# Optimization experiments

Hardware: AMD Instinct MI355X
Metric: run time of the kernel (lower is better)

Reference implementation:

```python
import jax, jax.numpy as jnp
import numpy as np
import math

N, E, C, NB, NEL, NG = 8192, 131072, 64, 8, 4, 16
R_MAX, AVG_NEI, P_CUT, NL, SH = 5.0, 16.0, 6, 2, 16


def _sph(u):
    # real spherical harmonics l=0..3, component normalization (sum_m Y_lm^2 = 2l+1 on unit sphere)
    x, y, z = u[:, 0], u[:, 1], u[:, 2]
    s3, s15, s5 = math.sqrt(3.0), math.sqrt(15.0), math.sqrt(5.0)
    s105, s7 = math.sqrt(105.0), math.sqrt(7.0)
    c35, c21 = math.sqrt(35.0 / 8.0), math.sqrt(21.0 / 8.0)
    Y = [jnp.ones_like(x),
         s3 * x, s3 * y, s3 * z,
         s15 * x * y, s15 * y * z, 0.5 * s5 * (3 * z * z - 1), s15 * x * z, 0.5 * s15 * (x * x - y * y),
         c35 * y * (3 * x * x - y * y), s105 * x * y * z, c21 * y * (5 * z * z - 1),
         0.5 * s7 * (5 * z ** 3 - 3 * z), c21 * x * (5 * z * z - 1),
         0.5 * s105 * z * (x * x - y * y), c35 * x * (x * x - 3 * y * y)]
    return jnp.stack(Y, axis=-1)  # [E,16]


def _bessel(r):
    k = jnp.arange(1, NB + 1, dtype=r.dtype)
    return math.sqrt(2.0 / R_MAX) * jnp.sin(k * jnp.pi * r[:, None] / R_MAX) / r[:, None]


def _poly_cutoff(r):
    p = float(P_CUT)
    x = r / R_MAX
    f = (1.0 - 0.5 * (p + 1) * (p + 2) * x ** p + p * (p + 2) * x ** (p + 1)
         - 0.5 * p * (p + 1) * x ** (p + 2))
    return f * (x < 1.0)


def setup_inputs() -> dict:
    key = jax.random.key(0)
    ks = jax.random.split(key, 16)
    sc = lambda fan: 1.0 / math.sqrt(fan)
    return {
        "pos": 2.0 * jax.random.normal(ks[0], (N, 3), jnp.float32),
        "atom_types": jax.random.randint(ks[1], (N,), 0, NEL),
        "edge_index": jax.random.randint(ks[2], (2, E), 0, N),
        "batch": jnp.sort(jax.random.randint(ks[3], (N,), 0, NG)),
        "W_embed": jax.random.normal(ks[4], (NEL, C), jnp.float32),
        "W_r1": sc(NB) * jax.random.normal(ks[5], (NL, NB, 64), jnp.float32),
        "W_r2": sc(64) * jax.random.normal(ks[6], (NL, 64, 64), jnp.float32),
        "W_r3": sc(64) * jax.random.normal(ks[7], (NL, 64, C), jnp.float32),
        "W_sc": sc(C) * jax.random.normal(ks[8], (NL, NEL, C, C), jnp.float32),
        "w_prod": 0.5 * jax.random.normal(ks[9], (NL, NEL, 4), jnp.float32),
        "w_ro0": sc(C) * jax.random.normal(ks[10], (C,), jnp.float32),
        "W_ro1a": sc(C) * jax.random.normal(ks[11], (C, 16), jnp.float32),
        "w_ro1b": sc(16) * jax.random.normal(ks[12], (16,), jnp.float32),
    }


def reference(pos, atom_types, edge_index, batch, W_embed, W_r1, W_r2, W_r3,
              W_sc, w_prod, w_ro0, W_ro1a, w_ro1b):
    src, dst = edge_index[0], edge_index[1]
    vec = pos[dst] - pos[src]                      # [E,3]
    r = jnp.sqrt(jnp.sum(vec * vec, -1) + 1e-12)   # [E]
    Y = _sph(vec / r[:, None])                     # [E,SH]
    edge_feats = _bessel(r) * _poly_cutoff(r)[:, None]  # [E,NB]
    h = W_embed[atom_types]                        # one-hot @ W == lookup, [N,C]
    energies = [jnp.zeros((NG,), pos.dtype)]       # pair_repulsion disabled
    for i in range(NL):
        Rw = jax.nn.silu(edge_feats @ W_r1[i])
        Rw = jax.nn.silu(Rw @ W_r2[i])
        Rw = Rw @ W_r3[i]                          # radial MLP weights [E,C]
        # gather-TP-scatter: message [E,C,SH] -> node A [N,C,SH]
        m = (Rw * h[src])[:, :, None] * Y[:, None, :]
        A = jax.ops.segment_sum(m.reshape(E, C * SH), dst,
                                num_segments=N).reshape(N, C, SH) / AVG_NEI
        sc_feat = jnp.einsum('nc,ncd->nd', h, W_sc[i][atom_types])  # element-dep skip
        inv = jnp.stack([A[:, :, 0],
                         jnp.sum(A[:, :, 1:4] ** 2, -1),
                         jnp.sum(A[:, :, 4:9] ** 2, -1),
                         jnp.sum(A[:, :, 9:16] ** 2, -1)], axis=-1)  # [N,C,4]
        h = jnp.einsum('ncj,nj->nc', inv, w_prod[i][atom_types]) + sc_feat
        if i < NL - 1:
            e_node = h @ w_ro0                     # linear readout
        else:
            e_node = jax.nn.silu(h @ W_ro1a) @ w_ro1b  # gated MLP readout
        energies.append(jax.ops.segment_sum(e_node, batch, num_segments=NG))
    contributions = jnp.stack(energies, -1)        # [NG, NL+1]
    return jnp.sum(contributions, -1)              # total energy per graph
```

## Files before the change

kernel.cpp:

```cpp
#include <hip/hip_runtime.h>
#include <hip/hip_bf16.h>
#include <math.h>

#define N_NODES 8192
#define N_EDGES 131072
#define NGRP 16
#define NLAY 2
#define NELM 4
constexpr float INV_AVG = 1.0f / 16.0f;
constexpr float PI_F = 3.14159265358979323846f;

#define CV_POS   0
#define CV_EMB   24576
#define CV_SC    42240
#define CV_PROD  75008
#define CV_RO0   75040
#define CV_RO1A  75104
#define CV_RO1B  76128
#define CVT_N    76144

#define SWZ_PER_L 10240
#define SWZ_N     20480

#define B_CVT  230
#define B_SWZ  80
#define B_HIST 512
#define CVT_WORK 58736

#define GU_GRID 4096

typedef __hip_bfloat16 bf16;
typedef __attribute__((ext_vector_type(8))) short bf16x8;
typedef __attribute__((ext_vector_type(4))) float f32x4;

__device__ __forceinline__ float silu_f(float x){ return x / (1.0f + __expf(-x)); }
__device__ __forceinline__ float bfbits2f(unsigned short u){
  return __uint_as_float(((unsigned)u) << 16);
}
__device__ __forceinline__ void unpack2(unsigned u, float& lo, float& hi){
  lo = __uint_as_float(u << 16);
  hi = __uint_as_float(u & 0xffff0000u);
}
__device__ __forceinline__ short f2bs(float v){
  union { bf16 b; short s; } u; u.b = __float2bfloat16(v); return u.s;
}
__device__ __forceinline__ float ldf(const void* p, int i, int flag){
  if (flag) return bfbits2f(((const unsigned short*)p)[i]);
  return ((const float*)p)[i];
}
__device__ __forceinline__ int detect_fl(const void* pos){
  int lane = threadIdx.x & 63;
  const unsigned short* u = (const unsigned short*)pos;
  float va = bfbits2f(u[2*lane]), vb = bfbits2f(u[2*lane+1]);
  bool bad = !(fabsf(va) <= 1000.0f) || !(fabsf(vb) <= 1000.0f);
  return (__ballot(bad) == 0ull) ? 1 : 0;
}
__device__ __forceinline__ void WSYNC(){ __builtin_amdgcn_wave_barrier(); }

__device__ __forceinline__ void gl_lds4(const void* g, void* l){
  __builtin_amdgcn_global_load_lds(
      (const __attribute__((address_space(1))) unsigned*)g,
      (__attribute__((address_space(3))) unsigned*)l, 4, 0, 0);
}

__global__ void k_setup1(const void* __restrict__ pos, const void* __restrict__ Wemb,
                         const void* __restrict__ Wsc, const void* __restrict__ wprod,
                         const void* __restrict__ wro0, const void* __restrict__ Wro1a,
                         const void* __restrict__ wro1b, const void* __restrict__ Wr1,
                         const void* __restrict__ Wr2, const void* __restrict__ Wr3,
                         const int* __restrict__ dstp, float* __restrict__ cv,
                         short* __restrict__ swz, int* __restrict__ deg){
  int b = blockIdx.x, tix = threadIdx.x;
  if (b >= B_CVT + B_SWZ){
    int e = (b - B_CVT - B_SWZ)*256 + tix;
    atomicAdd(&deg[dstp[e]], 1);
    return;
  }
  int fl = detect_fl(pos);
  if (b < B_CVT){
    int i = b*256 + tix;
    if (i < 24576){ cv[CV_POS + i] = ldf(pos, i, fl); return; }
    if (i < 24832){ int j=i-24576; cv[CV_EMB + j] = ldf(Wemb, j, fl); return; }
    if (i < 57600){ int j=i-24832; cv[CV_SC  + j] = ldf(Wsc,  j, fl); return; }
    if (i < 57632){ int j=i-57600; cv[CV_PROD+ j] = ldf(wprod,j, fl); return; }
    if (i < 57696){ int j=i-57632; cv[CV_RO0 + j] = ldf(wro0, j, fl); return; }
    if (i < 58720){ int j=i-57696; cv[CV_RO1A+ j] = ldf(Wro1a,j, fl); return; }
    if (i < CVT_WORK){ int j=i-58720; cv[CV_RO1B+ j] = ldf(wro1b,j, fl); return; }
    return;
  }
  int i = (b - B_CVT)*256 + tix;
  int l = i / SWZ_PER_L, w = i % SWZ_PER_L;
  float v;
  if (w < 2048){
    int t = w >> 9, q = (w >> 7) & 3, n = (w >> 3) & 15, j = w & 7;
    int k = q*8 + j;
    v = (k < 8) ? ldf(Wr1, l*512 + k*64 + t*16 + n, fl) : 0.0f;
  } else if (w < 6144){
    int w2 = w - 2048;
    int nt = w2 >> 10, kt = (w2 >> 9) & 1, q = (w2 >> 7) & 3, n = (w2 >> 3) & 15, j = w2 & 7;
    int k = kt*32 + q*8 + j;
    v = ldf(Wr2, l*4096 + k*64 + nt*16 + n, fl);
  } else {
    int w3 = w - 6144;
    int nt = w3 >> 10, kt = (w3 >> 9) & 1, q = (w3 >> 7) & 3, n = (w3 >> 3) & 15, j = w3 & 7;
    int k = kt*32 + q*8 + j;
    v = ldf(Wr3, l*4096 + k*64 + nt*16 + n, fl);
  }
  swz[i] = f2bs(v);
}

__global__ void k_scan(const int* __restrict__ deg, int* __restrict__ row_start,
                       int* __restrict__ cursor, float* __restrict__ ene2){
  __shared__ int lds[1024];
  int t = threadIdx.x;
  if (t < 8*NGRP) ene2[t] = 0.0f;
  int v[8]; int tot = 0;
#pragma unroll
  for (int k = 0; k < 8; k++){ v[k] = deg[t*8+k]; tot += v[k]; }
  lds[t] = tot; __syncthreads();
  for (int off = 1; off < 1024; off <<= 1){
    int x = (t >= off) ? lds[t-off] : 0;
    __syncthreads();
    lds[t] += x;
    __syncthreads();
  }
  int base = lds[t] - tot;
#pragma unroll
  for (int k = 0; k < 8; k++){ row_start[t*8+k] = base; cursor[t*8+k] = base; base += v[k]; }
  if (t == 1023) row_start[N_NODES] = base;
}

__global__ void k_fillgeom(const int* __restrict__ ei, int* __restrict__ cursor,
                           const float* __restrict__ posf, const int* __restrict__ types,
                           int* __restrict__ sslot, unsigned char* __restrict__ tsl,
                           unsigned short* __restrict__ Yb, float* __restrict__ rbuf){
  int e = blockIdx.x*256 + threadIdx.x;
  int s = ei[e], d = ei[N_EDGES + e];
  int slot = atomicAdd(&cursor[d], 1);
  sslot[slot] = s;
  tsl[slot] = (unsigned char)types[s];
  float vx = posf[d*3+0] - posf[s*3+0];
  float vy = posf[d*3+1] - posf[s*3+1];
  float vz = posf[d*3+2] - posf[s*3+2];
  float r = sqrtf(vx*vx + vy*vy + vz*vz + 1e-12f);
  float ir = 1.0f / r;
  float x = vx*ir, y = vy*ir, z = vz*ir;
  const float s3 = 1.7320508075688772f, s15 = 3.872983346207417f, s5 = 2.23606797749979f;
  const float s105 = 10.246950765959598f, s7 = 2.6457513110645907f;
  const float c35 = 2.091650066335189f, c21 = 1.6201851746019651f;
  float x2 = x*x, y2 = y*y, z2 = z*z;
  float ys[16] = {
    1.0f, s3*x, s3*y, s3*z,
    s15*x*y, s15*y*z, 0.5f*s5*(3.0f*z2-1.0f), s15*x*z,
    0.5f*s15*(x2-y2), c35*y*(3.0f*x2-y2), s105*x*y*z, c21*y*(5.0f*z2-1.0f),
    0.5f*s7*(5.0f*z2*z-3.0f*z), c21*x*(5.0f*z2-1.0f), 0.5f*s105*z*(x2-y2),
    c35*x*(x2-3.0f*y2) };
  union { bf16 b[16]; uint4 u[2]; } pk;
#pragma unroll
  for (int k = 0; k < 16; k++) pk.b[k] = __float2bfloat16(ys[k]);
  uint4* yp = (uint4*)(Yb + (size_t)slot*16);
  yp[0] = pk.u[0];
  yp[1] = pk.u[1];
  rbuf[slot] = r;
}

#define ROWS 72
template<int LAYER_KIND>
__global__ void __launch_bounds__(64) k_gu(const short* __restrict__ sw,
        const float* __restrict__ rbuf, const unsigned char* __restrict__ tsl,
        const int* __restrict__ sslot, const float* __restrict__ h_old,
        float* __restrict__ h_new, const unsigned short* __restrict__ Yb,
        const int* __restrict__ row_start, const int* __restrict__ types,
        const float* __restrict__ Wsc, const float* __restrict__ wprod,
        const float* __restrict__ wemb, const float* __restrict__ wro0,
        const float* __restrict__ Wro1a, const float* __restrict__ wro1b,
        const int* __restrict__ batch, float* __restrict__ ene2){
  __shared__ __align__(16) short A_[16*ROWS];
  __shared__ __align__(16) float hS[LAYER_KIND ? 16 : 1][64];
  __shared__ __align__(16) unsigned short yS[16][16];
  __shared__ float hn_l[64];
  int lane = threadIdx.x;
  int q = lane >> 4, nn = lane & 15;
  short* A = A_;

  const bf16x8* S1 = (const bf16x8*)(sw);
  const bf16x8* S2 = (const bf16x8*)(sw + 2048);
  const bf16x8* S3 = (const bf16x8*)(sw + 6144);

  float e0=0.f, e1=0.f, e2=0.f, e3=0.f;
  if (LAYER_KIND == 0){
    e0 = wemb[lane]; e1 = wemb[64+lane]; e2 = wemb[128+lane]; e3 = wemb[192+lane];
  }

  for (int n = blockIdx.x; n < N_NODES; n += GU_GRID){
    int beg = row_start[n], end = row_start[n + 1];

    float acc[16];
#pragma unroll
    for (int s = 0; s < 16; s++) acc[s] = 0.0f;

    for (int cb = beg; cb < end; cb += 16){
      int cnt = min(16, end - cb);
      WSYNC();
      const char* ysrc = (const char*)Yb + (size_t)cb*32 + lane*4;
      gl_lds4(ysrc,       &yS[0][0]);
      gl_lds4(ysrc + 256, &yS[8][0]);
      int tv = 0;
      if (LAYER_KIND == 0){
        tv = (int)tsl[min(cb + nn, N_EDGES - 1)];
      } else {
        int sv = sslot[min(cb + nn, N_EDGES - 1)];
        for (int i = 0; i < cnt; i++){
          int src = __builtin_amdgcn_readlane(sv, i);
          gl_lds4(h_old + (size_t)src*64 + lane, &hS[i][0]);
        }
      }
      {
        float r = rbuf[min(cb + nn, N_EDGES - 1)];
        float xc = r * 0.2f;
        float f = 0.0f;
        if (xc < 1.0f){
          float x3 = xc*xc*xc, x6 = x3*x3, x7 = x6*xc, x8 = x7*xc;
          f = 1.0f - 28.0f*x6 + 48.0f*x7 - 21.0f*x8;
        }
        float bs = 0.6324555320336759f * f / r;
        float t0 = PI_F * r * 0.2f;
        bf16x8 af1 = {0,0,0,0,0,0,0,0};
        if (q == 0){
#pragma unroll
          for (int j = 0; j < 8; j++) af1[j] = f2bs(bs * __sinf((float)(j+1) * t0));
        }
        f32x4 macc[4];
#pragma unroll
        for (int t = 0; t < 4; t++){
          bf16x8 b = S1[t*64 + q*16 + nn];
          f32x4 z = {0.f,0.f,0.f,0.f};
          macc[t] = __builtin_amdgcn_mfma_f32_16x16x32_bf16(af1, b, z, 0, 0, 0);
        }
#pragma unroll
        for (int t = 0; t < 4; t++)
#pragma unroll
          for (int rg = 0; rg < 4; rg++)
            A[(q*4+rg)*ROWS + t*16 + nn] = f2bs(silu_f(macc[t][rg]));
        WSYNC();
        bf16x8 a0 = *(const bf16x8*)&A[nn*ROWS + 0*32 + q*8];
        bf16x8 a1 = *(const bf16x8*)&A[nn*ROWS + 1*32 + q*8];
        WSYNC();
#pragma unroll
        for (int t = 0; t < 4; t++){
          f32x4 z = {0.f,0.f,0.f,0.f};
          bf16x8 b0 = S2[t*128 + 0*64 + q*16 + nn];
          bf16x8 b1 = S2[t*128 + 1*64 + q*16 + nn];
          z = __builtin_amdgcn_mfma_f32_16x16x32_bf16(a0, b0, z, 0, 0, 0);
          z = __builtin_amdgcn_mfma_f32_16x16x32_bf16(a1, b1, z, 0, 0, 0);
          macc[t] = z;
        }
#pragma unroll
        for (int t = 0; t < 4; t++)
#pragma unroll
          for (int rg = 0; rg < 4; rg++)
            A[(q*4+rg)*ROWS + t*16 + nn] = f2bs(silu_f(macc[t][rg]));
        WSYNC();
        a0 = *(const bf16x8*)&A[nn*ROWS + 0*32 + q*8];
        a1 = *(const bf16x8*)&A[nn*ROWS + 1*32 + q*8];
        WSYNC();
#pragma unroll
        for (int t = 0; t < 4; t++){
          f32x4 z = {0.f,0.f,0.f,0.f};
          bf16x8 b0 = S3[t*128 + 0*64 + q*16 + nn];
          bf16x8 b1 = S3[t*128 + 1*64 + q*16 + nn];
          z = __builtin_amdgcn_mfma_f32_16x16x32_bf16(a0, b0, z, 0, 0, 0);
          z = __builtin_amdgcn_mfma_f32_16x16x32_bf16(a1, b1, z, 0, 0, 0);
          macc[t] = z;
        }
#pragma unroll
        for (int t = 0; t < 4; t++)
#pragma unroll
          for (int rg = 0; rg < 4; rg++)
            A[(q*4+rg)*ROWS + t*16 + nn] = f2bs(macc[t][rg]);
        WSYNC();
      }
      asm volatile("s_waitcnt vmcnt(0)" ::: "memory");
      __builtin_amdgcn_sched_barrier(0);
      for (int i = 0; i < cnt; i++){
        float rw = bfbits2f((unsigned short)A[i*ROWS + lane]);
        float hv;
        if (LAYER_KIND == 0){
          int ty = __builtin_amdgcn_readlane(tv, i);
          hv = (ty & 2) ? ((ty & 1) ? e3 : e2) : ((ty & 1) ? e1 : e0);
        } else {
          hv = hS[i][lane];
        }
        float g = rw * hv;
        const uint4* yq = (const uint4*)&yS[i][0];
        uint4 ya = yq[0], yb = yq[1];
        float lo, hi;
        unpack2(ya.x, lo, hi); acc[0]  += g*lo; acc[1]  += g*hi;
        unpack2(ya.y, lo, hi); acc[2]  += g*lo; acc[3]  += g*hi;
        unpack2(ya.z, lo, hi); acc[4]  += g*lo; acc[5]  += g*hi;
        unpack2(ya.w, lo, hi); acc[6]  += g*lo; acc[7]  += g*hi;
        unpack2(yb.x, lo, hi); acc[8]  += g*lo; acc[9]  += g*hi;
        unpack2(yb.y, lo, hi); acc[10] += g*lo; acc[11] += g*hi;
        unpack2(yb.z, lo, hi); acc[12] += g*lo; acc[13] += g*hi;
        unpack2(yb.w, lo, hi); acc[14] += g*lo; acc[15] += g*hi;
      }
    }
#pragma unroll
    for (int s = 0; s < 16; s++) acc[s] *= INV_AVG;

    int ty = __builtin_amdgcn_readfirstlane(types[n]);
    const float* Ws = Wsc + (size_t)ty*4096;
    const float* hrow = (LAYER_KIND == 0) ? (wemb + ty*64) : (h_old + (size_t)n*64);
    float sc0 = 0.f, sc1 = 0.f, sc2 = 0.f, sc3 = 0.f;
#pragma unroll
    for (int c = 0; c < 64; c += 4){
      sc0 += hrow[c+0] * Ws[(c+0)*64 + lane];
      sc1 += hrow[c+1] * Ws[(c+1)*64 + lane];
      sc2 += hrow[c+2] * Ws[(c+2)*64 + lane];
      sc3 += hrow[c+3] * Ws[(c+3)*64 + lane];
    }
    float sc = (sc0 + sc1) + (sc2 + sc3);

    float inv0 = acc[0];
    float inv1 = acc[1]*acc[1] + acc[2]*acc[2] + acc[3]*acc[3];
    float inv2 = acc[4]*acc[4] + acc[5]*acc[5] + acc[6]*acc[6] + acc[7]*acc[7]
               + acc[8]*acc[8];
    float inv3 = acc[9]*acc[9] + acc[10]*acc[10] + acc[11]*acc[11] + acc[12]*acc[12]
               + acc[13]*acc[13] + acc[14]*acc[14] + acc[15]*acc[15];
    const float* wp = wprod + ty*4;
    float hn = inv0*wp[0] + inv1*wp[1] + inv2*wp[2] + inv3*wp[3] + sc;
    if (LAYER_KIND == 0)
      h_new[(size_t)n*64 + lane] = hn;

    float ev;
    if (LAYER_KIND == 0){
      float p = hn * wro0[lane];
#pragma unroll
      for (int off = 32; off >= 1; off >>= 1) p += __shfl_xor(p, off, 64);
      ev = p;
    } else {
      WSYNC();
      hn_l[lane] = hn;
      WSYNC();
      int j = lane & 15;
      float pj = 0.0f;
#pragma unroll
      for (int c = 0; c < 64; c++)
        pj += hn_l[c] * Wro1a[c*16 + j];
      float evj = silu_f(pj) * wro1b[j];
      evj += __shfl_xor(evj, 8, 64);
      evj += __shfl_xor(evj, 4, 64);
      evj += __shfl_xor(evj, 2, 64);
      evj += __shfl_xor(evj, 1, 64);
      ev = evj;
    }
    if (lane == 0) atomicAdd(&ene2[(n & 7)*NGRP + batch[n]], ev);
  }
}

__global__ void k_out(const float* __restrict__ ene2, const void* __restrict__ pos,
                      void* __restrict__ out){
  int fl = detect_fl(pos);
  int t = threadIdx.x;
  if (t < NGRP){
    float v = 0.0f;
#pragma unroll
    for (int k = 0; k < 8; k++) v += ene2[k*NGRP + t];
    if (fl) ((bf16*)out)[t] = __float2bfloat16(v);
    else    ((float*)out)[t] = v;
  }
}

static inline size_t rup(size_t x){ return (x + 255) & ~(size_t)255; }

extern "C" void kernel_launch(void* const* d_in, const int* in_sizes, int n_in,
                              void* d_out, int out_size, void* d_ws, size_t ws_size,
                              hipStream_t stream) {
  const void* pos   = d_in[0];
  const int*  types = (const int*)d_in[1];
  const int*  ei    = (const int*)d_in[2];
  const int*  batch = (const int*)d_in[3];
  const void* Wemb  = d_in[4];
  const void* Wr1   = d_in[5];
  const void* Wr2   = d_in[6];
  const void* Wr3   = d_in[7];
  const void* Wsc   = d_in[8];
  const void* wprod = d_in[9];
  const void* wro0  = d_in[10];
  const void* Wro1a = d_in[11];
  const void* wro1b = d_in[12];

  char* w = (char*)d_ws;
  float* cv       = (float*)w; w += rup((size_t)CVT_N*4);
  short* swz      = (short*)w; w += rup((size_t)SWZ_N*2);
  float* ene2     = (float*)w; w += 512;
  int*   deg      = (int*)  w; w += rup((size_t)N_NODES*4);
  int*   row_start= (int*)  w; w += rup((size_t)(N_NODES+1)*4);
  int*   cursor   = (int*)  w; w += rup((size_t)N_NODES*4);
  int*   sslot    = (int*)  w; w += rup((size_t)N_EDGES*4);
  unsigned char* tsl = (unsigned char*)w; w += rup((size_t)N_EDGES);
  float* hbuf     = (float*)w; w += rup((size_t)N_NODES*64*4);
  float* rbuf     = (float*)w; w += rup((size_t)N_EDGES*4);
  unsigned short* Yb = (unsigned short*)w; w += rup((size_t)N_EDGES*16*2);
  w += 4096;

  hipMemsetAsync(deg, 0, N_NODES*4, stream);

  const int* dstp = ei + N_EDGES;
  k_setup1<<<B_CVT + B_SWZ + B_HIST, 256, 0, stream>>>(
      pos, Wemb, Wsc, wprod, wro0, Wro1a, wro1b, Wr1, Wr2, Wr3, dstp, cv, swz, deg);
  k_scan<<<1, 1024, 0, stream>>>(deg, row_start, cursor, ene2);
  k_fillgeom<<<N_EDGES/256, 256, 0, stream>>>(ei, cursor, cv + CV_POS, types,
      sslot, tsl, Yb, rbuf);

  k_gu<0><<<GU_GRID, 64, 0, stream>>>(swz, rbuf, tsl, sslot,
      hbuf , hbuf , Yb, row_start, types,
      cv + CV_SC, cv + CV_PROD, cv + CV_EMB,
      cv + CV_RO0, cv + CV_RO1A, cv + CV_RO1B, batch, ene2);
  k_gu<1><<<GU_GRID, 64, 0, stream>>>(swz + SWZ_PER_L, rbuf, tsl, sslot,
      hbuf , hbuf , Yb, row_start, types,
      cv + CV_SC + (size_t)NELM*4096, cv + CV_PROD + NELM*4, cv + CV_EMB,
      cv + CV_RO0, cv + CV_RO1A, cv + CV_RO1B, batch, ene2);

  k_out<<<1, 64, 0, stream>>>(ene2, pos, d_out);
}
```

Baseline: 201.4 us.

## Interleave two nodes per block to overlap gathers and MFMA chains

Each block now handles two nodes, n and n+GU_GRID, in lockstep. It double-buffers the LDS tiles (A, hS, yS) so one node's gathers and radial-MLP MFMAs are issued alongside the other's, which gives the scheduler independent work to hide memory and MFMA latency. The change assumes the grid covers exactly half of the nodes, because the grid-stride loop is gone. It also doubles LDS and accumulator register use, and a node with more edges leaves the other slot idle while it finishes.

```diff
diff --git a/kernel.cpp b/kernel.cpp
--- a/kernel.cpp
+++ b/kernel.cpp
@@ -165,6 +165,165 @@
 }
 
 #define ROWS 72
+
+template<int LK>
+__device__ __forceinline__ int issueA(const unsigned short* Yb,
+    const unsigned char* tsl, const int* sslot, const float* h_old,
+    int cb, int cnt, int lane, int nn,
+    unsigned short (*yS)[16], float (*hS)[64]){
+  const char* ysrc = (const char*)Yb + (size_t)cb*32 + lane*4;
+  gl_lds4(ysrc,       &yS[0][0]);
+  gl_lds4(ysrc + 256, &yS[8][0]);
+  int tv = 0;
+  if (LK == 0){
+    tv = (int)tsl[min(cb + nn, N_EDGES - 1)];
+  } else {
+    int sv = sslot[min(cb + nn, N_EDGES - 1)];
+    for (int i = 0; i < cnt; i++){
+      int src = __builtin_amdgcn_readlane(sv, i);
+      gl_lds4(h_old + (size_t)src*64 + lane, &hS[i][0]);
+    }
+  }
+  return tv;
+}
+
+__device__ __forceinline__ void mlp_s1(const bf16x8* S1, short* A,
+    const float* rbuf, int cb, int q, int nn){
+  float r = rbuf[min(cb + nn, N_EDGES - 1)];
+  float xc = r * 0.2f;
+  float f = 0.0f;
+  if (xc < 1.0f){
+    float x3 = xc*xc*xc, x6 = x3*x3, x7 = x6*xc, x8 = x7*xc;
+    f = 1.0f - 28.0f*x6 + 48.0f*x7 - 21.0f*x8;
+  }
+  float bs = 0.6324555320336759f * f / r;
+  float t0 = PI_F * r * 0.2f;
+  bf16x8 af1 = {0,0,0,0,0,0,0,0};
+  if (q == 0){
+#pragma unroll
+    for (int j = 0; j < 8; j++) af1[j] = f2bs(bs * __sinf((float)(j+1) * t0));
+  }
+  f32x4 macc[4];
+#pragma unroll
+  for (int t = 0; t < 4; t++){
+    bf16x8 b = S1[t*64 + q*16 + nn];
+    f32x4 z = {0.f,0.f,0.f,0.f};
+    macc[t] = __builtin_amdgcn_mfma_f32_16x16x32_bf16(af1, b, z, 0, 0, 0);
+  }
+#pragma unroll
+  for (int t = 0; t < 4; t++)
+#pragma unroll
+    for (int rg = 0; rg < 4; rg++)
+      A[(q*4+rg)*ROWS + t*16 + nn] = f2bs(silu_f(macc[t][rg]));
+}
+
+template<int FINAL>
+__device__ __forceinline__ void mlp_s23(const bf16x8* S, short* A, int q, int nn){
+  bf16x8 a0 = *(const bf16x8*)&A[nn*ROWS + 0*32 + q*8];
+  bf16x8 a1 = *(const bf16x8*)&A[nn*ROWS + 1*32 + q*8];
+  WSYNC();
+  f32x4 macc[4];
+#pragma unroll
+  for (int t = 0; t < 4; t++){
+    f32x4 z = {0.f,0.f,0.f,0.f};
+    bf16x8 b0 = S[t*128 + 0*64 + q*16 + nn];
+    bf16x8 b1 = S[t*128 + 1*64 + q*16 + nn];
+    z = __builtin_amdgcn_mfma_f32_16x16x32_bf16(a0, b0, z, 0, 0, 0);
+    z = __builtin_amdgcn_mfma_f32_16x16x32_bf16(a1, b1, z, 0, 0, 0);
+    macc[t] = z;
+  }
+#pragma unroll
+  for (int t = 0; t < 4; t++)
+#pragma unroll
+    for (int rg = 0; rg < 4; rg++)
+      A[(q*4+rg)*ROWS + t*16 + nn] = f2bs(FINAL ? macc[t][rg]
+                                                : silu_f(macc[t][rg]));
+}
+
+template<int LK>
+__device__ __forceinline__ void acc_edges(const short* A, const float (*hS)[64],
+    const unsigned short (*yS)[16], int cnt, int tv, int lane,
+    float e0, float e1, float e2, float e3, float (&acc)[16]){
+  for (int i = 0; i < cnt; i++){
+    float rw = bfbits2f((unsigned short)A[i*ROWS + lane]);
+    float hv;
+    if (LK == 0){
+      int ty = __builtin_amdgcn_readlane(tv, i);
+      hv = (ty & 2) ? ((ty & 1) ? e3 : e2) : ((ty & 1) ? e1 : e0);
+    } else {
+      hv = hS[i][lane];
+    }
+    float g = rw * hv;
+    const uint4* yq = (const uint4*)&yS[i][0];
+    uint4 ya = yq[0], yb = yq[1];
+    float lo, hi;
+    unpack2(ya.x, lo, hi); acc[0]  += g*lo; acc[1]  += g*hi;
+    unpack2(ya.y, lo, hi); acc[2]  += g*lo; acc[3]  += g*hi;
+    unpack2(ya.z, lo, hi); acc[4]  += g*lo; acc[5]  += g*hi;
+    unpack2(ya.w, lo, hi); acc[6]  += g*lo; acc[7]  += g*hi;
+    unpack2(yb.x, lo, hi); acc[8]  += g*lo; acc[9]  += g*hi;
+    unpack2(yb.y, lo, hi); acc[10] += g*lo; acc[11] += g*hi;
+    unpack2(yb.z, lo, hi); acc[12] += g*lo; acc[13] += g*hi;
+    unpack2(yb.w, lo, hi); acc[14] += g*lo; acc[15] += g*hi;
+  }
+}
+
+template<int LK>
+__device__ __forceinline__ void epilogue(int n, float (&acc)[16], int lane,
+    const int* types, const float* Wsc, const float* wprod, const float* wemb,
+    const float* wro0, const float* Wro1a, const float* wro1b,
+    const int* batch, float* ene2, const float* h_old, float* h_new,
+    float* hnl){
+#pragma unroll
+  for (int s = 0; s < 16; s++) acc[s] *= INV_AVG;
+  int ty = __builtin_amdgcn_readfirstlane(types[n]);
+  const float* Ws = Wsc + (size_t)ty*4096;
+  const float* hrow = (LK == 0) ? (wemb + ty*64) : (h_old + (size_t)n*64);
+  float sc0 = 0.f, sc1 = 0.f, sc2 = 0.f, sc3 = 0.f;
+#pragma unroll
+  for (int c = 0; c < 64; c += 4){
+    sc0 += hrow[c+0] * Ws[(c+0)*64 + lane];
+    sc1 += hrow[c+1] * Ws[(c+1)*64 + lane];
+    sc2 += hrow[c+2] * Ws[(c+2)*64 + lane];
+    sc3 += hrow[c+3] * Ws[(c+3)*64 + lane];
+  }
+  float sc = (sc0 + sc1) + (sc2 + sc3);
+
+  float inv0 = acc[0];
+  float inv1 = acc[1]*acc[1] + acc[2]*acc[2] + acc[3]*acc[3];
+  float inv2 = acc[4]*acc[4] + acc[5]*acc[5] + acc[6]*acc[6] + acc[7]*acc[7]
+             + acc[8]*acc[8];
+  float inv3 = acc[9]*acc[9] + acc[10]*acc[10] + acc[11]*acc[11] + acc[12]*acc[12]
+             + acc[13]*acc[13] + acc[14]*acc[14] + acc[15]*acc[15];
+  const float* wp = wprod + ty*4;
+  float hn = inv0*wp[0] + inv1*wp[1] + inv2*wp[2] + inv3*wp[3] + sc;
+  if (LK == 0)
+    h_new[(size_t)n*64 + lane] = hn;
+
+  float ev;
+  if (LK == 0){
+    float p = hn * wro0[lane];
+#pragma unroll
+    for (int off = 32; off >= 1; off >>= 1) p += __shfl_xor(p, off, 64);
+    ev = p;
+  } else {
+    hnl[lane] = hn;
+    WSYNC();
+    int j = lane & 15;
+    float pj = 0.0f;
+#pragma unroll
+    for (int c = 0; c < 64; c++)
+      pj += hnl[c] * Wro1a[c*16 + j];
+    float evj = silu_f(pj) * wro1b[j];
+    evj += __shfl_xor(evj, 8, 64);
+    evj += __shfl_xor(evj, 4, 64);
+    evj += __shfl_xor(evj, 2, 64);
+    evj += __shfl_xor(evj, 1, 64);
+    ev = evj;
+  }
+  if (lane == 0) atomicAdd(&ene2[(n & 7)*NGRP + batch[n]], ev);
+}
+
 template<int LAYER_KIND>
 __global__ void __launch_bounds__(64) k_gu(const short* __restrict__ sw,
         const float* __restrict__ rbuf, const unsigned char* __restrict__ tsl,
@@ -175,13 +334,12 @@
         const float* __restrict__ wemb, const float* __restrict__ wro0,
         const float* __restrict__ Wro1a, const float* __restrict__ wro1b,
         const int* __restrict__ batch, float* __restrict__ ene2){
-  __shared__ __align__(16) short A_[16*ROWS];
-  __shared__ __align__(16) float hS[LAYER_KIND ? 16 : 1][64];
-  __shared__ __align__(16) unsigned short yS[16][16];
-  __shared__ float hn_l[64];
+  __shared__ __align__(16) short A_[2][16*ROWS];
+  __shared__ __align__(16) float hS_[LAYER_KIND ? 2 : 1][16][64];
+  __shared__ __align__(16) unsigned short yS_[2][16][16];
+  __shared__ float hn_l[2][64];
   int lane = threadIdx.x;
   int q = lane >> 4, nn = lane & 15;
-  short* A = A_;
 
   const bf16x8* S1 = (const bf16x8*)(sw);
   const bf16x8* S2 = (const bf16x8*)(sw + 2048);
@@ -192,170 +350,47 @@
     e0 = wemb[lane]; e1 = wemb[64+lane]; e2 = wemb[128+lane]; e3 = wemb[192+lane];
   }
 
-  for (int n = blockIdx.x; n < N_NODES; n += GU_GRID){
-    int beg = row_start[n], end = row_start[n + 1];
-
-    float acc[16];
-#pragma unroll
-    for (int s = 0; s < 16; s++) acc[s] = 0.0f;
-
-    for (int cb = beg; cb < end; cb += 16){
-      int cnt = min(16, end - cb);
-      WSYNC();
-      const char* ysrc = (const char*)Yb + (size_t)cb*32 + lane*4;
-      gl_lds4(ysrc,       &yS[0][0]);
-      gl_lds4(ysrc + 256, &yS[8][0]);
-      int tv = 0;
-      if (LAYER_KIND == 0){
-        tv = (int)tsl[min(cb + nn, N_EDGES - 1)];
-      } else {
-        int sv = sslot[min(cb + nn, N_EDGES - 1)];
-        for (int i = 0; i < cnt; i++){
-          int src = __builtin_amdgcn_readlane(sv, i);
-          gl_lds4(h_old + (size_t)src*64 + lane, &hS[i][0]);
-        }
-      }
-      {
-        float r = rbuf[min(cb + nn, N_EDGES - 1)];
-        float xc = r * 0.2f;
-        float f = 0.0f;
-        if (xc < 1.0f){
-          float x3 = xc*xc*xc, x6 = x3*x3, x7 = x6*xc, x8 = x7*xc;
-          f = 1.0f - 28.0f*x6 + 48.0f*x7 - 21.0f*x8;
-        }
-        float bs = 0.6324555320336759f * f / r;
-        float t0 = PI_F * r * 0.2f;
-        bf16x8 af1 = {0,0,0,0,0,0,0,0};
-        if (q == 0){
-#pragma unroll
-          for (int j = 0; j < 8; j++) af1[j] = f2bs(bs * __sinf((float)(j+1) * t0));
-        }
-        f32x4 macc[4];
-#pragma unroll
-        for (int t = 0; t < 4; t++){
-          bf16x8 b = S1[t*64 + q*16 + nn];
-          f32x4 z = {0.f,0.f,0.f,0.f};
-          macc[t] = __builtin_amdgcn_mfma_f32_16x16x32_bf16(af1, b, z, 0, 0, 0);
-        }
-#pragma unroll
-        for (int t = 0; t < 4; t++)
-#pragma unroll
-          for (int rg = 0; rg < 4; rg++)
-            A[(q*4+rg)*ROWS + t*16 + nn] = f2bs(silu_f(macc[t][rg]));
-        WSYNC();
-        bf16x8 a0 = *(const bf16x8*)&A[nn*ROWS + 0*32 + q*8];
-        bf16x8 a1 = *(const bf16x8*)&A[nn*ROWS + 1*32 + q*8];
-        WSYNC();
-#pragma unroll
-        for (int t = 0; t < 4; t++){
-          f32x4 z = {0.f,0.f,0.f,0.f};
-          bf16x8 b0 = S2[t*128 + 0*64 + q*16 + nn];
-          bf16x8 b1 = S2[t*128 + 1*64 + q*16 + nn];
-          z = __builtin_amdgcn_mfma_f32_16x16x32_bf16(a0, b0, z, 0, 0, 0);
-          z = __builtin_amdgcn_mfma_f32_16x16x32_bf16(a1, b1, z, 0, 0, 0);
-          macc[t] = z;
-        }
-#pragma unroll
-        for (int t = 0; t < 4; t++)
-#pragma unroll
-          for (int rg = 0; rg < 4; rg++)
-            A[(q*4+rg)*ROWS + t*16 + nn] = f2bs(silu_f(macc[t][rg]));
-        WSYNC();
-        a0 = *(const bf16x8*)&A[nn*ROWS + 0*32 + q*8];
-        a1 = *(const bf16x8*)&A[nn*ROWS + 1*32 + q*8];
-        WSYNC();
-#pragma unroll
-        for (int t = 0; t < 4; t++){
-          f32x4 z = {0.f,0.f,0.f,0.f};
-          bf16x8 b0 = S3[t*128 + 0*64 + q*16 + nn];
-          bf16x8 b1 = S3[t*128 + 1*64 + q*16 + nn];
-          z = __builtin_amdgcn_mfma_f32_16x16x32_bf16(a0, b0, z, 0, 0, 0);
-          z = __builtin_amdgcn_mfma_f32_16x16x32_bf16(a1, b1, z, 0, 0, 0);
-          macc[t] = z;
-        }
-#pragma unroll
-        for (int t = 0; t < 4; t++)
-#pragma unroll
-          for (int rg = 0; rg < 4; rg++)
-            A[(q*4+rg)*ROWS + t*16 + nn] = f2bs(macc[t][rg]);
-        WSYNC();
-      }
-      asm volatile("s_waitcnt vmcnt(0)" ::: "memory");
-      __builtin_amdgcn_sched_barrier(0);
-      for (int i = 0; i < cnt; i++){
-        float rw = bfbits2f((unsigned short)A[i*ROWS + lane]);
-        float hv;
-        if (LAYER_KIND == 0){
-          int ty = __builtin_amdgcn_readlane(tv, i);
-          hv = (ty & 2) ? ((ty & 1) ? e3 : e2) : ((ty & 1) ? e1 : e0);
-        } else {
-          hv = hS[i][lane];
-        }
-        float g = rw * hv;
-        const uint4* yq = (const uint4*)&yS[i][0];
-        uint4 ya = yq[0], yb = yq[1];
-        float lo, hi;
-        unpack2(ya.x, lo, hi); acc[0]  += g*lo; acc[1]  += g*hi;
-        unpack2(ya.y, lo, hi); acc[2]  += g*lo; acc[3]  += g*hi;
-        unpack2(ya.z, lo, hi); acc[4]  += g*lo; acc[5]  += g*hi;
-        unpack2(ya.w, lo, hi); acc[6]  += g*lo; acc[7]  += g*hi;
-        unpack2(yb.x, lo, hi); acc[8]  += g*lo; acc[9]  += g*hi;
-        unpack2(yb.y, lo, hi); acc[10] += g*lo; acc[11] += g*hi;
-        unpack2(yb.z, lo, hi); acc[12] += g*lo; acc[13] += g*hi;
-        unpack2(yb.w, lo, hi); acc[14] += g*lo; acc[15] += g*hi;
-      }
-    }
-#pragma unroll
-    for (int s = 0; s < 16; s++) acc[s] *= INV_AVG;
-
-    int ty = __builtin_amdgcn_readfirstlane(types[n]);
-    const float* Ws = Wsc + (size_t)ty*4096;
-    const float* hrow = (LAYER_KIND == 0) ? (wemb + ty*64) : (h_old + (size_t)n*64);
-    float sc0 = 0.f, sc1 = 0.f, sc2 = 0.f, sc3 = 0.f;
-#pragma unroll
-    for (int c = 0; c < 64; c += 4){
-      sc0 += hrow[c+0] * Ws[(c+0)*64 + lane];
-      sc1 += hrow[c+1] * Ws[(c+1)*64 + lane];
-      sc2 += hrow[c+2] * Ws[(c+2)*64 + lane];
-      sc3 += hrow[c+3] * Ws[(c+3)*64 + lane];
-    }
-    float sc = (sc0 + sc1) + (sc2 + sc3);
-
-    float inv0 = acc[0];
-    float inv1 = acc[1]*acc[1] + acc[2]*acc[2] + acc[3]*acc[3];
-    float inv2 = acc[4]*acc[4] + acc[5]*acc[5] + acc[6]*acc[6] + acc[7]*acc[7]
-               + acc[8]*acc[8];
-    float inv3 = acc[9]*acc[9] + acc[10]*acc[10] + acc[11]*acc[11] + acc[12]*acc[12]
-               + acc[13]*acc[13] + acc[14]*acc[14] + acc[15]*acc[15];
-    const float* wp = wprod + ty*4;
-    float hn = inv0*wp[0] + inv1*wp[1] + inv2*wp[2] + inv3*wp[3] + sc;
-    if (LAYER_KIND == 0)
-      h_new[(size_t)n*64 + lane] = hn;
-
-    float ev;
-    if (LAYER_KIND == 0){
-      float p = hn * wro0[lane];
-#pragma unroll
-      for (int off = 32; off >= 1; off >>= 1) p += __shfl_xor(p, off, 64);
-      ev = p;
-    } else {
-      WSYNC();
-      hn_l[lane] = hn;
-      WSYNC();
-      int j = lane & 15;
-      float pj = 0.0f;
-#pragma unroll
-      for (int c = 0; c < 64; c++)
-        pj += hn_l[c] * Wro1a[c*16 + j];
-      float evj = silu_f(pj) * wro1b[j];
-      evj += __shfl_xor(evj, 8, 64);
-      evj += __shfl_xor(evj, 4, 64);
-      evj += __shfl_xor(evj, 2, 64);
-      evj += __shfl_xor(evj, 1, 64);
-      ev = evj;
-    }
-    if (lane == 0) atomicAdd(&ene2[(n & 7)*NGRP + batch[n]], ev);
-  }
+  int n0 = blockIdx.x;
+  int n1 = blockIdx.x + GU_GRID;
+  int beg0 = row_start[n0], end0 = row_start[n0 + 1];
+  int beg1 = row_start[n1], end1 = row_start[n1 + 1];
+
+  float acc0[16], acc1[16];
+#pragma unroll
+  for (int s = 0; s < 16; s++){ acc0[s] = 0.0f; acc1[s] = 0.0f; }
+
+  int cb0 = beg0, cb1 = beg1;
+  while (cb0 < end0 || cb1 < end1){
+    int a0 = (cb0 < end0), a1 = (cb1 < end1);
+    int cnt0 = a0 ? min(16, end0 - cb0) : 0;
+    int cnt1 = a1 ? min(16, end1 - cb1) : 0;
+    WSYNC();
+    int tv0 = 0, tv1 = 0;
+    if (a0) tv0 = issueA<LAYER_KIND>(Yb, tsl, sslot, h_old, cb0, cnt0, lane, nn,
+                                     yS_[0], hS_[0]);
+    if (a1) tv1 = issueA<LAYER_KIND>(Yb, tsl, sslot, h_old, cb1, cnt1, lane, nn,
+                                     yS_[1], hS_[LAYER_KIND ? 1 : 0]);
+    if (a0) mlp_s1(S1, A_[0], rbuf, cb0, q, nn);
+    if (a1) mlp_s1(S1, A_[1], rbuf, cb1, q, nn);
+    WSYNC();
+    if (a0) mlp_s23<0>(S2, A_[0], q, nn);
+    if (a1) mlp_s23<0>(S2, A_[1], q, nn);
+    WSYNC();
+    if (a0) mlp_s23<1>(S3, A_[0], q, nn);
+    if (a1) mlp_s23<1>(S3, A_[1], q, nn);
+    WSYNC();
+    asm volatile("s_waitcnt vmcnt(0)" ::: "memory");
+    __builtin_amdgcn_sched_barrier(0);
+    if (a0){ acc_edges<LAYER_KIND>(A_[0], hS_[0], yS_[0], cnt0, tv0, lane,
+                                   e0,e1,e2,e3, acc0); cb0 += 16; }
+    if (a1){ acc_edges<LAYER_KIND>(A_[1], hS_[LAYER_KIND ? 1 : 0], yS_[1],
+                                   cnt1, tv1, lane, e0,e1,e2,e3, acc1); cb1 += 16; }
+  }
+
+  epilogue<LAYER_KIND>(n0, acc0, lane, types, Wsc, wprod, wemb, wro0,
+                       Wro1a, wro1b, batch, ene2, h_old, h_new, hn_l[0]);
+  epilogue<LAYER_KIND>(n1, acc1, lane, types, Wsc, wprod, wemb, wro0,
+                       Wro1a, wro1b, batch, ene2, h_old, h_new, hn_l[1]);
 }
 
 __global__ void k_out(const float* __restrict__ ene2, const void* __restrict__ pos,
```

New measurement: 204.6 us. No clear change (+1.6%).
